# Performance work log

Hardware: AMD Instinct MI355X
Metric: run time of the kernel (lower is better)

## Reference

```python
import jax, jax.numpy as jnp
import numpy as np

B, S, E, P, K, H = 32, 512, 1024, 256, 3, 8
KERNELS = 4  # conv repeated KERNELS times then averaged -> identical to a single conv


def setup_inputs() -> dict:
    key = jax.random.key(0)
    ks = jax.random.split(key, 8)
    sc = 0.02
    x = jax.random.normal(ks[0], (B, S, E), jnp.float32)
    # lengths must satisfy 3 <= l <= S-1 so slice [1:l+1] and conv length l-2 are valid
    seq_length = jax.random.randint(ks[1], (B,), 16, S - 1)
    proj_w = jax.random.normal(ks[2], (E, P), jnp.float32) * sc
    proj_b = jnp.zeros((P,), jnp.float32)
    conv_w = jax.random.normal(ks[3], (P, P, K), jnp.float32) * sc  # (out, in, width)
    conv_b = jnp.zeros((P,), jnp.float32)
    attn_w = jax.random.normal(ks[4], (P, H * S), jnp.float32) * sc
    attn_b = jnp.zeros((H * S,), jnp.float32)
    c1_w = jax.random.normal(ks[5], (P, P // 2), jnp.float32) * sc
    c1_b = jnp.zeros((P // 2,), jnp.float32)
    c2_w = jax.random.normal(ks[6], (P // 2, 2), jnp.float32) * sc
    c2_b = jnp.zeros((2,), jnp.float32)
    return dict(x=x, seq_length=seq_length, proj_w=proj_w, proj_b=proj_b,
                conv_w=conv_w, conv_b=conv_b, attn_w=attn_w, attn_b=attn_b,
                c1_w=c1_w, c1_b=c1_b, c2_w=c2_w, c2_b=c2_b)


def _forward(x, seq_length, proj_w, proj_b, conv_w, conv_b, attn_w, attn_b,
             c1_w, c1_b, c2_w, c2_b):
    # projection: (B,S,E) -> (B,S,P)
    proj = jnp.einsum('bse,ep->bsp', x, proj_w) + proj_b
    proj_pc = jnp.transpose(proj, (0, 2, 1))  # (B,P,S)
    # original convs each sample over slice [1:l+1]; conv is local, so conv the
    # full slice [1:] once and mask invalid tail positions per sample.
    conv = jax.lax.conv_general_dilated(
        proj_pc[:, :, 1:], conv_w, window_strides=(1,), padding='VALID',
        dimension_numbers=('NCH', 'OIH', 'NCH'))  # (B,P,S-K)
    conv = jax.nn.relu(conv + conv_b[None, :, None])
    # sum of KERNELS identical relu(conv) outputs divided by KERNELS == conv (identity)
    m = S - K  # conv output length over slice [1:]
    l = seq_length[:, None]  # (B,1)
    valid = jnp.arange(m)[None, :] < (l - (K - 1))  # output j valid iff j < l-2
    conv = jnp.where(valid[:, None, :], conv, 0.0)
    # pad: position 0 zero, conv outputs at 1..l-2, zeros after -> (B,P,S)
    rep_conv = jnp.zeros((B, P, S), conv.dtype).at[:, :, 1:1 + m].set(conv)
    rep_conv = jnp.transpose(rep_conv, (0, 2, 1))  # (B,S,P)
    # attention: logits (B,S,H*S), softmax over the FULL H*S axis (original dim=1)
    logits = jnp.einsum('bsp,pk->bsk', rep_conv, attn_w) + attn_b
    attn = jax.nn.softmax(logits, axis=-1).reshape(B, S, H, S)
    # per sample: mean over heads, sum over query rows -> weights over key pos q
    w = attn.sum(axis=(1, 2)) / H  # (B,S)
    rep_attn = jnp.einsum('bq,bqp->bp', w, rep_conv)  # (B,P)
    h = jnp.einsum('bp,ph->bh', rep_attn, c1_w) + c1_b
    h = jnp.where(h > 0, h, 0.01 * h)  # LeakyReLU(0.01)
    cls = jnp.einsum('bh,hc->bc', h, c2_w) + c2_b
    return jax.nn.softmax(cls, axis=-1)


def reference(x, seq_length, proj_w, proj_b, conv_w, conv_b, attn_w, attn_b,
              c1_w, c1_b, c2_w, c2_b):
    probs = _forward(x, seq_length, proj_w, proj_b, conv_w, conv_b,
                     attn_w, attn_b, c1_w, c1_b, c2_w, c2_b)
    return probs, jnp.argmax(probs, axis=1)
```

## Files before the change

### kernel.cpp

```cpp
#include <hip/hip_runtime.h>

#define B_ 32
#define S_ 512
#define E_ 1024
#define P_ 256
#define HH 8

typedef __attribute__((ext_vector_type(8))) short bf16x8;
typedef __attribute__((ext_vector_type(8))) unsigned short us8;
typedef __attribute__((ext_vector_type(4))) unsigned short us4;
typedef __attribute__((ext_vector_type(16))) float f32x16;

static __device__ __forceinline__ unsigned short f2bf(float f) {
  union { float f; unsigned int u; } v;
  v.f = f;
  unsigned int r = (v.u + 0x7FFFu + ((v.u >> 16) & 1u)) >> 16;
  return (unsigned short)r;
}
static __device__ __forceinline__ float bf2f(unsigned short u) {
  union { unsigned int u; float f; } v;
  v.u = ((unsigned int)u) << 16;
  return v.f;
}

__global__ __launch_bounds__(256) void k_wtT(const float* __restrict__ cw,
                                             unsigned short* __restrict__ wtT) {
  int o = blockIdx.x, k = blockIdx.y, i = threadIdx.x;
  wtT[o * 768 + k * 256 + i] = f2bf(cw[o * 768 + i * 3 + k]);
}

__global__ __launch_bounds__(256) void k_pwT(const float* __restrict__ pw,
                                             unsigned short* __restrict__ pwT) {
  __shared__ float T[32][33];
  int n0 = blockIdx.x * 32;
  int k0 = blockIdx.y * 32;
  int tx = threadIdx.x & 31, ty = threadIdx.x >> 5;
#pragma unroll
  for (int i = 0; i < 4; i++)
    T[ty + i * 8][tx] = pw[(k0 + ty + i * 8) * P_ + n0 + tx];
  __syncthreads();
#pragma unroll
  for (int i = 0; i < 4; i++)
    pwT[(size_t)(n0 + ty + i * 8) * E_ + k0 + tx] = f2bf(T[tx][ty + i * 8]);
}

__global__ __launch_bounds__(256) void k_awT(const float* __restrict__ aw,
                                             unsigned short* __restrict__ awT) {
  __shared__ float T[32][33];
  int j0 = blockIdx.x * 32;
  int k0 = blockIdx.y * 32;
  int tx = threadIdx.x & 31, ty = threadIdx.x >> 5;
#pragma unroll
  for (int i = 0; i < 4; i++)
    T[ty + i * 8][tx] = aw[(k0 + ty + i * 8) * 4096 + j0 + tx];
  __syncthreads();
#pragma unroll
  for (int i = 0; i < 4; i++)
    awT[(size_t)(j0 + ty + i * 8) * 256 + k0 + tx] = f2bf(T[tx][ty + i * 8]);
}

__global__ __launch_bounds__(256) void k_swz(const unsigned short* __restrict__ src,
                                             unsigned short* __restrict__ dst,
                                             int K, int NK) {
  int g = blockIdx.x, kc = blockIdx.y * 4 + (threadIdx.x >> 6);
  int l = threadIdx.x & 63;
  us8 v = *(const us8*)(src + (size_t)(g * 32 + (l & 31)) * K + kc * 16 + (l >> 5) * 8);
  *(us8*)(dst + ((size_t)g * NK + kc) * 512 + l * 8) = v;
}

__global__ __launch_bounds__(256) void k_zero(float* __restrict__ p) {
  p[blockIdx.x * 256 + threadIdx.x] = 0.f;
}

__global__ __launch_bounds__(256) void k_proj_mfma(const float* __restrict__ x,
                                                   const unsigned short* __restrict__ pwB,
                                                   const float* __restrict__ pb,
                                                   unsigned short* __restrict__ proj16) {
  __shared__ unsigned short As[16 * 64 * 8];
  const int m0 = blockIdx.x * 64;
  const int t = threadIdx.x;
  const int w = t >> 6, lane = t & 63, ln31 = lane & 31, kh = lane >> 5;
  const int c0 = w * 64;

  f32x16 acc00, acc01, acc10, acc11;
#pragma unroll
  for (int r = 0; r < 16; r++) { acc00[r] = 0.f; acc01[r] = 0.f; acc10[r] = 0.f; acc11[r] = 0.f; }

  const unsigned short* bp0 = pwB + (size_t)(2 * w) * 64 * 512 + lane * 8;
  const unsigned short* bp1 = bp0 + (size_t)64 * 512;

  for (int kc = 0; kc < E_; kc += 128) {
#pragma unroll
    for (int i = 0; i < 8; i++) {
      int c = t + i * 256;
      int row = c >> 5, pos = c & 31;
      float4 v = *(const float4*)(x + (size_t)(m0 + row) * E_ + kc + pos * 4);
      us4 h;
      h[0] = f2bf(v.x); h[1] = f2bf(v.y); h[2] = f2bf(v.z); h[3] = f2bf(v.w);
      *(us4*)&As[((pos >> 1) * 64 + row) * 8 + (pos & 1) * 4] = h;
    }
    __syncthreads();
    const int kcs = kc >> 4;
#pragma unroll
    for (int kk = 0; kk < 8; kk++) {
      bf16x8 a0 = *(const bf16x8*)&As[((2 * kk + kh) * 64 + ln31) * 8];
      bf16x8 a1 = *(const bf16x8*)&As[((2 * kk + kh) * 64 + 32 + ln31) * 8];
      bf16x8 b0 = *(const bf16x8*)(bp0 + (size_t)(kcs + kk) * 512);
      bf16x8 b1 = *(const bf16x8*)(bp1 + (size_t)(kcs + kk) * 512);
      acc00 = __builtin_amdgcn_mfma_f32_32x32x16_bf16(a0, b0, acc00, 0, 0, 0);
      acc01 = __builtin_amdgcn_mfma_f32_32x32x16_bf16(a0, b1, acc01, 0, 0, 0);
      acc10 = __builtin_amdgcn_mfma_f32_32x32x16_bf16(a1, b0, acc10, 0, 0, 0);
      acc11 = __builtin_amdgcn_mfma_f32_32x32x16_bf16(a1, b1, acc11, 0, 0, 0);
    }
    __syncthreads();
  }
  float pb0 = pb[c0 + ln31], pb1 = pb[c0 + 32 + ln31];
#pragma unroll
  for (int r = 0; r < 16; r++) {
    int rl = (r & 3) + 8 * (r >> 2) + 4 * kh;
    size_t g0 = (size_t)(m0 + rl) * P_;
    size_t g1 = (size_t)(m0 + 32 + rl) * P_;
    proj16[g0 + c0 + ln31]      = f2bf(acc00[r] + pb0);
    proj16[g0 + c0 + 32 + ln31] = f2bf(acc01[r] + pb1);
    proj16[g1 + c0 + ln31]      = f2bf(acc10[r] + pb0);
    proj16[g1 + c0 + 32 + ln31] = f2bf(acc11[r] + pb1);
  }
}

__global__ __launch_bounds__(256) void k_conv_mfma(const unsigned short* __restrict__ proj16,
                                                   const unsigned short* __restrict__ wtB,
                                                   const float* __restrict__ cb,
                                                   const int* __restrict__ seq,
                                                   unsigned short* __restrict__ rep16) {
  __shared__ unsigned short As[32 * 66 * 8];
  const int m0 = blockIdx.x * 64;
  const int bb = m0 >> 9, s0 = m0 & 511;
  const int t = threadIdx.x;
  const int w = t >> 6, lane = t & 63, ln31 = lane & 31, kh = lane >> 5;
  const int c0 = w * 64;

#pragma unroll
  for (int i = 0; i < 9; i++) {
    int c = t + i * 256;
    if (c < 2112) {
      int row = c >> 5, kk2 = c & 31;
      us8 v = {0, 0, 0, 0, 0, 0, 0, 0};
      if (s0 + row <= 511)
        v = *(const us8*)(proj16 + (size_t)(bb * S_ + s0 + row) * P_ + kk2 * 8);
      *(us8*)&As[(kk2 * 66 + row) * 8] = v;
    }
  }
  __syncthreads();

  f32x16 acc00, acc01, acc10, acc11;
#pragma unroll
  for (int r = 0; r < 16; r++) { acc00[r] = 0.f; acc01[r] = 0.f; acc10[r] = 0.f; acc11[r] = 0.f; }

  const unsigned short* bb0 = wtB + (size_t)(2 * w) * 48 * 512 + lane * 8;
  const unsigned short* bb1 = bb0 + (size_t)48 * 512;

#pragma unroll
  for (int k = 0; k < 3; k++) {
#pragma unroll
    for (int kk = 0; kk < 16; kk++) {
      bf16x8 a0 = *(const bf16x8*)&As[((2 * kk + kh) * 66 + k + ln31) * 8];
      bf16x8 a1 = *(const bf16x8*)&As[((2 * kk + kh) * 66 + k + 32 + ln31) * 8];
      bf16x8 b0 = *(const bf16x8*)(bb0 + (size_t)(k * 16 + kk) * 512);
      bf16x8 b1 = *(const bf16x8*)(bb1 + (size_t)(k * 16 + kk) * 512);
      acc00 = __builtin_amdgcn_mfma_f32_32x32x16_bf16(a0, b0, acc00, 0, 0, 0);
      acc01 = __builtin_amdgcn_mfma_f32_32x32x16_bf16(a0, b1, acc01, 0, 0, 0);
      acc10 = __builtin_amdgcn_mfma_f32_32x32x16_bf16(a1, b0, acc10, 0, 0, 0);
      acc11 = __builtin_amdgcn_mfma_f32_32x32x16_bf16(a1, b1, acc11, 0, 0, 0);
    }
  }

  int l = seq[bb];
  float cb0 = cb[c0 + ln31], cb1 = cb[c0 + 32 + ln31];
#pragma unroll
  for (int r = 0; r < 16; r++) {
    int rl = (r & 3) + 8 * (r >> 2) + 4 * kh;
    int s_a = s0 + rl, s_b = s0 + 32 + rl;
    float ma = (s_a >= 1 && s_a <= 509 && s_a < l - 1) ? 1.f : 0.f;
    float mb = (s_b >= 1 && s_b <= 509 && s_b < l - 1) ? 1.f : 0.f;
    size_t g0 = (size_t)(m0 + rl) * P_;
    size_t g1 = (size_t)(m0 + 32 + rl) * P_;
    rep16[g0 + c0 + ln31]      = f2bf(fmaxf(acc00[r] + cb0, 0.f) * ma);
    rep16[g0 + c0 + 32 + ln31] = f2bf(fmaxf(acc01[r] + cb1, 0.f) * ma);
    rep16[g1 + c0 + ln31]      = f2bf(fmaxf(acc10[r] + cb0, 0.f) * mb);
    rep16[g1 + c0 + 32 + ln31] = f2bf(fmaxf(acc11[r] + cb1, 0.f) * mb);
  }
}

__global__ __launch_bounds__(256, 2) void k_attn_mfma(const unsigned short* __restrict__ repF,
                                                      const unsigned short* __restrict__ awB,
                                                      const float* __restrict__ ab,
                                                      unsigned short* __restrict__ E16,
                                                      float* __restrict__ Z) {
  const int m0 = blockIdx.x * 64;
  const int q0 = blockIdx.y * 128;
  const int t = threadIdx.x;
  const int w = t >> 6;
  const int lane = t & 63;
  const int ln31 = lane & 31;
  const int kh = lane >> 5;

  bf16x8 ar0[16], ar1[16];
  {
    const unsigned short* abase = repF + ((size_t)(m0 >> 5) * 16) * 512 + lane * 8;
#pragma unroll
    for (int kc = 0; kc < 16; kc++) {
      ar0[kc] = *(const bf16x8*)(abase + (size_t)kc * 512);
      ar1[kc] = *(const bf16x8*)(abase + (size_t)(16 + kc) * 512);
    }
  }

  const int qgidx = (q0 >> 5) + w;
  const int qcol = qgidx * 32 + ln31;

  float ef0[16], ef1[16];
#pragma unroll
  for (int r = 0; r < 16; r++) { ef0[r] = 0.f; ef1[r] = 0.f; }

#pragma unroll 1
  for (int h = 0; h < HH; h++) {
    const unsigned short* bh = awB + ((size_t)(h * 16 + qgidx) * 16) * 512 + lane * 8;
    f32x16 acc0, acc1;
#pragma unroll
    for (int r = 0; r < 16; r++) { acc0[r] = 0.f; acc1[r] = 0.f; }

#pragma unroll
    for (int kc = 0; kc < 16; kc++) {
      bf16x8 b = *(const bf16x8*)(bh + (size_t)kc * 512);
      acc0 = __builtin_amdgcn_mfma_f32_32x32x16_bf16(ar0[kc], b, acc0, 0, 0, 0);
      acc1 = __builtin_amdgcn_mfma_f32_32x32x16_bf16(ar1[kc], b, acc1, 0, 0, 0);
    }
    float bias = ab[h * 512 + qcol];
#pragma unroll
    for (int r = 0; r < 16; r++) {
      ef0[r] += __expf(acc0[r] + bias);
      ef1[r] += __expf(acc1[r] + bias);
    }
  }

#pragma unroll
  for (int r = 0; r < 16; r++) {
    int rl = (r & 3) + 8 * (r >> 2) + 4 * kh;
    E16[(size_t)(m0 + rl) * 512 + qcol]      = f2bf(ef0[r]);
    E16[(size_t)(m0 + 32 + rl) * 512 + qcol] = f2bf(ef1[r]);
  }

#pragma unroll
  for (int r = 0; r < 16; r++) {
    float z0 = ef0[r];
    float z1 = ef1[r];
#pragma unroll
    for (int st = 16; st >= 1; st >>= 1) {
      z0 += __shfl_xor(z0, st, 64);
      z1 += __shfl_xor(z1, st, 64);
    }
    if (ln31 == 0) {
      int rl = (r & 3) + 8 * (r >> 2) + 4 * kh;
      atomicAdd(&Z[m0 + rl], z0);
      atomicAdd(&Z[m0 + 32 + rl], z1);
    }
  }
}

__global__ __launch_bounds__(512) void k_w(const unsigned short* __restrict__ E16,
                                           const float* __restrict__ Z,
                                           float* __restrict__ wB) {
  __shared__ float rZ[64];
  int b = blockIdx.x, c = blockIdx.y, t = threadIdx.x;
  int s0 = c * 64;
  if (t < 64) rZ[t] = 1.0f / Z[b * 512 + s0 + t];
  __syncthreads();
  float acc = 0.f;
#pragma unroll 8
  for (int s = 0; s < 64; s++)
    acc += bf2f(E16[(size_t)(b * 512 + s0 + s) * 512 + t]) * rZ[s];
  atomicAdd(&wB[b * 512 + t], acc * (1.0f / HH));
}

__global__ __launch_bounds__(256) void k_final_a(const unsigned short* __restrict__ rep16,
                                                 const float* __restrict__ wB,
                                                 float* __restrict__ repA) {
  __shared__ float wS[64];
  int b = blockIdx.x, qc = blockIdx.y, t = threadIdx.x;
  if (t < 64) wS[t] = wB[b * 512 + qc * 64 + t];
  __syncthreads();
  float acc = 0.f;
  const unsigned short* base = rep16 + (size_t)(b * 512 + qc * 64) * 256 + t;
#pragma unroll 8
  for (int q = 0; q < 64; q++) acc += wS[q] * bf2f(base[(size_t)q * 256]);
  atomicAdd(&repA[b * 256 + t], acc);
}

__global__ __launch_bounds__(128) void k_final_b(const float* __restrict__ repA,
                                                 const float* __restrict__ c1w,
                                                 const float* __restrict__ c1b,
                                                 const float* __restrict__ c2w,
                                                 const float* __restrict__ c2b,
                                                 float* __restrict__ out) {
  __shared__ float hS[128];
  __shared__ float clsS[2];
  int b = blockIdx.x, t = threadIdx.x;
  float acc = c1b[t];
  for (int p = 0; p < 256; p++) acc += repA[b * 256 + p] * c1w[p * 128 + t];
  hS[t] = acc > 0.f ? acc : 0.01f * acc;
  __syncthreads();
  if (t < 2) {
    float a2 = c2b[t];
    for (int j = 0; j < 128; j++) a2 += hS[j] * c2w[j * 2 + t];
    clsS[t] = a2;
  }
  __syncthreads();
  if (t == 0) {
    float c0 = clsS[0], c1 = clsS[1];
    float m = fmaxf(c0, c1);
    float e0 = __expf(c0 - m), e1 = __expf(c1 - m);
    float inv = 1.0f / (e0 + e1);
    float p0 = e0 * inv, p1 = e1 * inv;
    out[b * 2 + 0] = p0;
    out[b * 2 + 1] = p1;
    out[B_ * 2 + b] = (p1 > p0) ? 1.0f : 0.0f;
  }
}

extern "C" void kernel_launch(void* const* d_in, const int* in_sizes, int n_in,
                              void* d_out, int out_size, void* d_ws, size_t ws_size,
                              hipStream_t stream) {
  const float* x   = (const float*)d_in[0];
  const int*   seq = (const int*)d_in[1];
  const float* pw  = (const float*)d_in[2];
  const float* pb  = (const float*)d_in[3];
  const float* cw  = (const float*)d_in[4];
  const float* cb  = (const float*)d_in[5];
  const float* aw  = (const float*)d_in[6];
  const float* ab  = (const float*)d_in[7];
  const float* c1w = (const float*)d_in[8];
  const float* c1b = (const float*)d_in[9];
  const float* c2w = (const float*)d_in[10];
  const float* c2b = (const float*)d_in[11];
  float* out = (float*)d_out;

  char* ws = (char*)d_ws;
  unsigned short* proj16 = (unsigned short*)(ws);
  unsigned short* E16    = (unsigned short*)(ws);
  unsigned short* rep16  = (unsigned short*)(ws + (size_t)16777216);
  unsigned short* pwT    = (unsigned short*)(ws + (size_t)25165824);
  unsigned short* wtT    = (unsigned short*)(ws + (size_t)25690112);
  unsigned short* awT    = (unsigned short*)(ws + (size_t)26083328);
  float*          Z      = (float*)(ws + (size_t)28180480);
  float*          wB     = (float*)(ws + (size_t)28246016);
  float*          repA   = (float*)(ws + (size_t)28311552);
  unsigned short* awB    = (unsigned short*)(ws + (size_t)28377088);
  unsigned short* pwB    = (unsigned short*)(ws + (size_t)30474240);
  unsigned short* wtB    = (unsigned short*)(ws + (size_t)30998528);
  unsigned short* repF   = (unsigned short*)(ws + (size_t)31391744);

  k_zero<<<160, 256, 0, stream>>>(Z);
  k_wtT<<<dim3(256, 3), 256, 0, stream>>>(cw, wtT);
  k_pwT<<<dim3(8, 32), 256, 0, stream>>>(pw, pwT);
  k_awT<<<dim3(128, 8), 256, 0, stream>>>(aw, awT);
  k_swz<<<dim3(128, 4), 256, 0, stream>>>(awT, awB, 256, 16);
  k_swz<<<dim3(8, 16), 256, 0, stream>>>(pwT, pwB, 1024, 64);
  k_swz<<<dim3(8, 12), 256, 0, stream>>>(wtT, wtB, 768, 48);

  k_proj_mfma<<<256, 256, 0, stream>>>(x, pwB, pb, proj16);
  k_conv_mfma<<<256, 256, 0, stream>>>(proj16, wtB, cb, seq, rep16);
  k_swz<<<dim3(512, 4), 256, 0, stream>>>(rep16, repF, 256, 16);
  k_attn_mfma<<<dim3(256, 4), 256, 0, stream>>>(repF, awB, ab, E16, Z);
  k_w<<<dim3(32, 8), 512, 0, stream>>>(E16, Z, wB);
  k_final_a<<<dim3(32, 8), 256, 0, stream>>>(rep16, wB, repA);
  k_final_b<<<32, 128, 0, stream>>>(repA, c1w, c1b, c2w, c2b, out);
}
```

Before: 249.5 us.

## Switch attention GEMM to 16x16x32 MFMA and fuse weight transpose-swizzle kernels

The attention logits kernel moves from 32x32x16 to 16x16x32 bf16 MFMA tiles, with operands swizzled into a new 16-row fragment layout. The exp-sum reduction now uses 16-lane shuffles. The weight preprocessing (transpose, bf16 convert, swizzle) is merged into single kernels per weight, which removes intermediate buffers and several launches. The new MFMA shape changes register use and the number of instructions issued, which may change occupancy and throughput either way.

```diff
diff --git a/kernel.cpp b/kernel.cpp
--- a/kernel.cpp
+++ b/kernel.cpp
@@ -10,6 +10,7 @@
 typedef __attribute__((ext_vector_type(8))) unsigned short us8;
 typedef __attribute__((ext_vector_type(4))) unsigned short us4;
 typedef __attribute__((ext_vector_type(16))) float f32x16;
+typedef __attribute__((ext_vector_type(4))) float f32x4;
 
 static __device__ __forceinline__ unsigned short f2bf(float f) {
   union { float f; unsigned int u; } v;
@@ -23,49 +24,52 @@
   return v.f;
 }
 
-__global__ __launch_bounds__(256) void k_wtT(const float* __restrict__ cw,
-                                             unsigned short* __restrict__ wtT) {
-  int o = blockIdx.x, k = blockIdx.y, i = threadIdx.x;
-  wtT[o * 768 + k * 256 + i] = f2bf(cw[o * 768 + i * 3 + k]);
-}
-
-__global__ __launch_bounds__(256) void k_pwT(const float* __restrict__ pw,
-                                             unsigned short* __restrict__ pwT) {
-  __shared__ float T[32][33];
-  int n0 = blockIdx.x * 32;
-  int k0 = blockIdx.y * 32;
-  int tx = threadIdx.x & 31, ty = threadIdx.x >> 5;
-#pragma unroll
-  for (int i = 0; i < 4; i++)
-    T[ty + i * 8][tx] = pw[(k0 + ty + i * 8) * P_ + n0 + tx];
-  __syncthreads();
-#pragma unroll
-  for (int i = 0; i < 4; i++)
-    pwT[(size_t)(n0 + ty + i * 8) * E_ + k0 + tx] = f2bf(T[tx][ty + i * 8]);
-}
-
-__global__ __launch_bounds__(256) void k_awT(const float* __restrict__ aw,
-                                             unsigned short* __restrict__ awT) {
-  __shared__ float T[32][33];
-  int j0 = blockIdx.x * 32;
-  int k0 = blockIdx.y * 32;
-  int tx = threadIdx.x & 31, ty = threadIdx.x >> 5;
-#pragma unroll
-  for (int i = 0; i < 4; i++)
-    T[ty + i * 8][tx] = aw[(k0 + ty + i * 8) * 4096 + j0 + tx];
-  __syncthreads();
-#pragma unroll
-  for (int i = 0; i < 4; i++)
-    awT[(size_t)(j0 + ty + i * 8) * 256 + k0 + tx] = f2bf(T[tx][ty + i * 8]);
-}
-
-__global__ __launch_bounds__(256) void k_swz(const unsigned short* __restrict__ src,
-                                             unsigned short* __restrict__ dst,
-                                             int K, int NK) {
+__global__ __launch_bounds__(256) void k_pwB(const float* __restrict__ pw,
+                                             unsigned short* __restrict__ dst) {
   int g = blockIdx.x, kc = blockIdx.y * 4 + (threadIdx.x >> 6);
   int l = threadIdx.x & 63;
-  us8 v = *(const us8*)(src + (size_t)(g * 32 + (l & 31)) * K + kc * 16 + (l >> 5) * 8);
-  *(us8*)(dst + ((size_t)g * NK + kc) * 512 + l * 8) = v;
+  int n = g * 32 + (l & 31);
+  int kbase = kc * 16 + (l >> 5) * 8;
+  us8 v;
+#pragma unroll
+  for (int j = 0; j < 8; j++) v[j] = f2bf(pw[(size_t)(kbase + j) * P_ + n]);
+  *(us8*)(dst + ((size_t)g * 64 + kc) * 512 + l * 8) = v;
+}
+
+__global__ __launch_bounds__(256) void k_wtB(const float* __restrict__ cw,
+                                             unsigned short* __restrict__ dst) {
+  int g = blockIdx.x, kidx = blockIdx.y * 4 + (threadIdx.x >> 6);
+  int l = threadIdx.x & 63;
+  int o = g * 32 + (l & 31);
+  int xb = kidx * 16 + (l >> 5) * 8;
+  us8 v;
+#pragma unroll
+  for (int j = 0; j < 8; j++) {
+    int x = xb + j;
+    int k = x >> 8, i = x & 255;
+    v[j] = f2bf(cw[(size_t)o * 768 + i * 3 + k]);
+  }
+  *(us8*)(dst + ((size_t)g * 48 + kidx) * 512 + l * 8) = v;
+}
+
+__global__ __launch_bounds__(256) void k_awB16(const float* __restrict__ aw,
+                                               unsigned short* __restrict__ dst) {
+  int g = blockIdx.x, ks = blockIdx.y * 4 + (threadIdx.x >> 6);
+  int l = threadIdx.x & 63;
+  int j0 = g * 16 + (l & 15);
+  int kbase = ks * 32 + (l >> 4) * 8;
+  us8 v;
+#pragma unroll
+  for (int j = 0; j < 8; j++) v[j] = f2bf(aw[(size_t)(kbase + j) * 4096 + j0]);
+  *(us8*)(dst + ((size_t)g * 8 + ks) * 512 + l * 8) = v;
+}
+
+__global__ __launch_bounds__(256) void k_swz16(const unsigned short* __restrict__ src,
+                                               unsigned short* __restrict__ dst) {
+  int g = blockIdx.x, ks = blockIdx.y * 4 + (threadIdx.x >> 6);
+  int l = threadIdx.x & 63;
+  us8 v = *(const us8*)(src + (size_t)(g * 16 + (l & 15)) * 256 + ks * 32 + (l >> 4) * 8);
+  *(us8*)(dst + ((size_t)g * 8 + ks) * 512 + l * 8) = v;
 }
 
 __global__ __launch_bounds__(256) void k_zero(float* __restrict__ p) {
@@ -199,71 +203,70 @@
   const int m0 = blockIdx.x * 64;
   const int q0 = blockIdx.y * 128;
   const int t = threadIdx.x;
-  const int w = t >> 6;
-  const int lane = t & 63;
-  const int ln31 = lane & 31;
-  const int kh = lane >> 5;
-
-  bf16x8 ar0[16], ar1[16];
+  const int w = t >> 6, lane = t & 63;
+  const int ln15 = lane & 15, l4 = lane >> 4;
+
+  bf16x8 ar[4][8];
   {
-    const unsigned short* abase = repF + ((size_t)(m0 >> 5) * 16) * 512 + lane * 8;
-#pragma unroll
-    for (int kc = 0; kc < 16; kc++) {
-      ar0[kc] = *(const bf16x8*)(abase + (size_t)kc * 512);
-      ar1[kc] = *(const bf16x8*)(abase + (size_t)(16 + kc) * 512);
-    }
-  }
-
-  const int qgidx = (q0 >> 5) + w;
-  const int qcol = qgidx * 32 + ln31;
-
-  float ef0[16], ef1[16];
-#pragma unroll
-  for (int r = 0; r < 16; r++) { ef0[r] = 0.f; ef1[r] = 0.f; }
+    const unsigned short* abase = repF + (size_t)(m0 >> 4) * 8 * 512 + lane * 8;
+#pragma unroll
+    for (int rt = 0; rt < 4; rt++)
+#pragma unroll
+      for (int ks = 0; ks < 8; ks++)
+        ar[rt][ks] = *(const bf16x8*)(abase + (size_t)(rt * 8 + ks) * 512);
+  }
+
+  const int qg = (q0 >> 5) + w;
+
+  f32x4 ef[8];
+#pragma unroll
+  for (int i = 0; i < 8; i++) ef[i] = (f32x4){0.f, 0.f, 0.f, 0.f};
 
 #pragma unroll 1
   for (int h = 0; h < HH; h++) {
-    const unsigned short* bh = awB + ((size_t)(h * 16 + qgidx) * 16) * 512 + lane * 8;
-    f32x16 acc0, acc1;
-#pragma unroll
-    for (int r = 0; r < 16; r++) { acc0[r] = 0.f; acc1[r] = 0.f; }
-
-#pragma unroll
-    for (int kc = 0; kc < 16; kc++) {
-      bf16x8 b = *(const bf16x8*)(bh + (size_t)kc * 512);
-      acc0 = __builtin_amdgcn_mfma_f32_32x32x16_bf16(ar0[kc], b, acc0, 0, 0, 0);
-      acc1 = __builtin_amdgcn_mfma_f32_32x32x16_bf16(ar1[kc], b, acc1, 0, 0, 0);
-    }
-    float bias = ab[h * 512 + qcol];
-#pragma unroll
-    for (int r = 0; r < 16; r++) {
-      ef0[r] += __expf(acc0[r] + bias);
-      ef1[r] += __expf(acc1[r] + bias);
-    }
-  }
-
-#pragma unroll
-  for (int r = 0; r < 16; r++) {
-    int rl = (r & 3) + 8 * (r >> 2) + 4 * kh;
-    E16[(size_t)(m0 + rl) * 512 + qcol]      = f2bf(ef0[r]);
-    E16[(size_t)(m0 + 32 + rl) * 512 + qcol] = f2bf(ef1[r]);
-  }
-
-#pragma unroll
-  for (int r = 0; r < 16; r++) {
-    float z0 = ef0[r];
-    float z1 = ef1[r];
-#pragma unroll
-    for (int st = 16; st >= 1; st >>= 1) {
-      z0 += __shfl_xor(z0, st, 64);
-      z1 += __shfl_xor(z1, st, 64);
-    }
-    if (ln31 == 0) {
-      int rl = (r & 3) + 8 * (r >> 2) + 4 * kh;
-      atomicAdd(&Z[m0 + rl], z0);
-      atomicAdd(&Z[m0 + 32 + rl], z1);
-    }
-  }
+    const unsigned short* bh = awB + (size_t)(h * 32 + qg * 2) * 8 * 512 + lane * 8;
+    f32x4 acc[8];
+#pragma unroll
+    for (int i = 0; i < 8; i++) acc[i] = (f32x4){0.f, 0.f, 0.f, 0.f};
+#pragma unroll
+    for (int ks = 0; ks < 8; ks++) {
+      bf16x8 b0 = *(const bf16x8*)(bh + (size_t)ks * 512);
+      bf16x8 b1 = *(const bf16x8*)(bh + (size_t)(8 + ks) * 512);
+#pragma unroll
+      for (int rt = 0; rt < 4; rt++) {
+        acc[rt * 2 + 0] = __builtin_amdgcn_mfma_f32_16x16x32_bf16(ar[rt][ks], b0, acc[rt * 2 + 0], 0, 0, 0);
+        acc[rt * 2 + 1] = __builtin_amdgcn_mfma_f32_16x16x32_bf16(ar[rt][ks], b1, acc[rt * 2 + 1], 0, 0, 0);
+      }
+    }
+    float bias0 = ab[h * 512 + qg * 32 + ln15];
+    float bias1 = ab[h * 512 + qg * 32 + 16 + ln15];
+#pragma unroll
+    for (int rt = 0; rt < 4; rt++)
+#pragma unroll
+      for (int r = 0; r < 4; r++) {
+        ef[rt * 2 + 0][r] += __expf(acc[rt * 2 + 0][r] + bias0);
+        ef[rt * 2 + 1][r] += __expf(acc[rt * 2 + 1][r] + bias1);
+      }
+  }
+
+#pragma unroll
+  for (int rt = 0; rt < 4; rt++)
+#pragma unroll
+    for (int r = 0; r < 4; r++) {
+      int row = m0 + rt * 16 + l4 * 4 + r;
+      E16[(size_t)row * 512 + qg * 32 + ln15]      = f2bf(ef[rt * 2 + 0][r]);
+      E16[(size_t)row * 512 + qg * 32 + 16 + ln15] = f2bf(ef[rt * 2 + 1][r]);
+    }
+
+#pragma unroll
+  for (int rt = 0; rt < 4; rt++)
+#pragma unroll
+    for (int r = 0; r < 4; r++) {
+      float z = ef[rt * 2 + 0][r] + ef[rt * 2 + 1][r];
+#pragma unroll
+      for (int st = 8; st >= 1; st >>= 1) z += __shfl_xor(z, st, 64);
+      if (ln15 == 0) atomicAdd(&Z[m0 + rt * 16 + l4 * 4 + r], z);
+    }
 }
 
 __global__ __launch_bounds__(512) void k_w(const unsigned short* __restrict__ E16,
@@ -347,28 +350,22 @@
   unsigned short* proj16 = (unsigned short*)(ws);
   unsigned short* E16    = (unsigned short*)(ws);
   unsigned short* rep16  = (unsigned short*)(ws + (size_t)16777216);
-  unsigned short* pwT    = (unsigned short*)(ws + (size_t)25165824);
-  unsigned short* wtT    = (unsigned short*)(ws + (size_t)25690112);
-  unsigned short* awT    = (unsigned short*)(ws + (size_t)26083328);
-  float*          Z      = (float*)(ws + (size_t)28180480);
-  float*          wB     = (float*)(ws + (size_t)28246016);
-  float*          repA   = (float*)(ws + (size_t)28311552);
-  unsigned short* awB    = (unsigned short*)(ws + (size_t)28377088);
-  unsigned short* pwB    = (unsigned short*)(ws + (size_t)30474240);
-  unsigned short* wtB    = (unsigned short*)(ws + (size_t)30998528);
-  unsigned short* repF   = (unsigned short*)(ws + (size_t)31391744);
+  unsigned short* repF   = (unsigned short*)(ws + (size_t)25165824);
+  unsigned short* awB    = (unsigned short*)(ws + (size_t)33554432);
+  unsigned short* pwB    = (unsigned short*)(ws + (size_t)35651584);
+  unsigned short* wtB    = (unsigned short*)(ws + (size_t)36175872);
+  float*          Z      = (float*)(ws + (size_t)36569088);
+  float*          wB     = (float*)(ws + (size_t)36634624);
+  float*          repA   = (float*)(ws + (size_t)36700160);
 
   k_zero<<<160, 256, 0, stream>>>(Z);
-  k_wtT<<<dim3(256, 3), 256, 0, stream>>>(cw, wtT);
-  k_pwT<<<dim3(8, 32), 256, 0, stream>>>(pw, pwT);
-  k_awT<<<dim3(128, 8), 256, 0, stream>>>(aw, awT);
-  k_swz<<<dim3(128, 4), 256, 0, stream>>>(awT, awB, 256, 16);
-  k_swz<<<dim3(8, 16), 256, 0, stream>>>(pwT, pwB, 1024, 64);
-  k_swz<<<dim3(8, 12), 256, 0, stream>>>(wtT, wtB, 768, 48);
+  k_pwB<<<dim3(8, 16), 256, 0, stream>>>(pw, pwB);
+  k_wtB<<<dim3(8, 12), 256, 0, stream>>>(cw, wtB);
+  k_awB16<<<dim3(256, 2), 256, 0, stream>>>(aw, awB);
 
   k_proj_mfma<<<256, 256, 0, stream>>>(x, pwB, pb, proj16);
   k_conv_mfma<<<256, 256, 0, stream>>>(proj16, wtB, cb, seq, rep16);
-  k_swz<<<dim3(512, 4), 256, 0, stream>>>(rep16, repF, 256, 16);
+  k_swz16<<<dim3(1024, 2), 256, 0, stream>>>(rep16, repF);
   k_attn_mfma<<<dim3(256, 4), 256, 0, stream>>>(repF, awB, ab, E16, Z);
   k_w<<<dim3(32, 8), 512, 0, stream>>>(E16, Z, wB);
   k_final_a<<<dim3(32, 8), 256, 0, stream>>>(rep16, wB, repA);
```

Result: faster. 237.4 us (-4.9%).
